# Optimization experiments

Measured on AMD Instinct MI355X. Metric: run time of the kernel, lower is better.

The kernel has to match this reference:

```python
import jax, jax.numpy as jnp
import numpy as np

N_NODES = 100000
N_RELS = 500
N_EDGES = 1000000
IN_DIM = 64
OUT_DIM = 64
BN_EPS = 1e-5


def _bn(v, gamma, beta):
    # BatchNorm1d in training mode: batch mean / biased variance
    m = jnp.mean(v, axis=0)
    var = jnp.var(v, axis=0)
    return (v - m) * jax.lax.rsqrt(var + BN_EPS) * gamma + beta


def setup_inputs() -> dict:
    key = jax.random.key(0)
    ks = jax.random.split(key, 12)
    inp = {
        "x": jax.random.normal(ks[0], (N_NODES, IN_DIM), dtype=jnp.float32),
        "r": jax.random.normal(ks[1], (N_RELS, IN_DIM), dtype=jnp.float32),
        "que_context": jax.random.normal(ks[2], (OUT_DIM,), dtype=jnp.float32),
        "edge_index": jax.random.randint(ks[3], (2, N_EDGES), 0, N_NODES),
        "edge_attr": jax.random.randint(ks[4], (N_EDGES,), 0, N_RELS),
        "edge_type": jax.random.randint(ks[5], (N_EDGES,), 0, N_RELS),
        # mess_trans: Linear(2*in_dim -> out_dim)
        "W_m": jax.random.normal(ks[6], (OUT_DIM, 2 * IN_DIM), dtype=jnp.float32) * 0.05,
        "b_m": jnp.zeros((OUT_DIM,), dtype=jnp.float32),
        # atten_weight: [2*out_dim] (stored as [1, 2*out_dim] in torch)
        "atten_w": jax.random.normal(ks[7], (2 * OUT_DIM,), dtype=jnp.float32) * 0.1,
        # rel_trans: Linear(in_dim -> out_dim)
        "W_r": jax.random.normal(ks[8], (OUT_DIM, IN_DIM), dtype=jnp.float32) * 0.05,
        "b_r": jnp.zeros((OUT_DIM,), dtype=jnp.float32),
        # batchnorm affine params
        "e_gamma": jnp.ones((OUT_DIM,), dtype=jnp.float32),
        "e_beta": jnp.zeros((OUT_DIM,), dtype=jnp.float32),
        "r_gamma": jnp.ones((OUT_DIM,), dtype=jnp.float32),
        "r_beta": jnp.zeros((OUT_DIM,), dtype=jnp.float32),
    }
    return inp


def reference(x, r, que_context, edge_index, edge_attr, edge_type,
              W_m, b_m, atten_w, W_r, b_r, e_gamma, e_beta, r_gamma, r_beta):
    src = edge_index[0]  # [E]
    tgt = edge_index[1]  # [E]

    # gather source-node and edge-relation embeddings, linear message transform
    source_embeds = x[src]            # [E, in_dim]
    edge_rel_embeds = r[edge_attr]    # [E, in_dim]
    messages = jnp.concatenate([source_embeds, edge_rel_embeds], axis=1) @ W_m.T + b_m  # [E, out_dim]

    # edge-wise attention score: <atten_w, [messages ; que_context]>
    # split dot product to avoid materializing the concat
    aw_m, aw_q = atten_w[:OUT_DIM], atten_w[OUT_DIM:]
    atten = messages @ aw_m + jnp.dot(aw_q, que_context)  # [E]
    atten = jnp.exp(jnp.tanh(atten))

    # scatter-sum normalization (softmax-like over incoming edges)
    coeffs_sum = jax.ops.segment_sum(atten, tgt, num_segments=N_NODES)  # [N]
    weights = atten / coeffs_sum[tgt]                                   # [E]

    # weighted scatter-sum aggregation
    x_new = jax.ops.segment_sum(messages * weights[:, None], tgt, num_segments=N_NODES)  # [N, out_dim]
    x_new = jnp.tanh(_bn(x_new, e_gamma, e_beta))  # dropout = identity (eval)

    r_new = jnp.tanh(_bn(r @ W_r.T + b_r, r_gamma, r_beta))
    return (x_new, r_new)
```

## Files before the change

kernel.cpp:

```cpp
#include <hip/hip_runtime.h>
#include <hip/hip_fp16.h>

#define N_NODES 100000
#define N_RELS  500
#define N_EDGES 1000000
#define SRCMASK 131071

#define OFF_C     0
#define OFF_SUMS  64
#define OFF_SUMSQ 128
#define OFF_RSUM  320
#define OFF_RSQ   384
#define OFF_SR    576
#define OFF_RP    1088
#define OFF_SX    33152
#define OFF_DEG   133152
#define OFF_OFF   233216
#define OFF_META  333248
#define OFF_PRH   2333248
#define OFF_PXH   2349280
#define OFF_ACCH  5549280
#define OFF_PART  8749280

typedef _Float16 h8 __attribute__((ext_vector_type(8)));
typedef float f4 __attribute__((ext_vector_type(4)));

__global__ void __launch_bounds__(256) k_rel(const float* __restrict__ r, const float* __restrict__ Wm,
                                             const float* __restrict__ Wr, const float* __restrict__ br,
                                             const float* __restrict__ aw, const float* __restrict__ bm,
                                             const float* __restrict__ que, float* __restrict__ ws) {
    __shared__ float wm[64][65];
    __shared__ float wr[64][65];
    __shared__ float awl[64];
    int tid = threadIdx.x;
    for (int i = tid; i < 4096; i += 256) {
        int row = i >> 6, col = i & 63;
        wm[row][col] = Wm[row * 128 + 64 + col];
        wr[row][col] = Wr[row * 64 + col];
    }
    if (tid < 64) awl[tid] = aw[tid];
    __syncthreads();
    int lane = tid & 63, wv = tid >> 6;
    int i = blockIdx.x * 4 + wv;
    float rv = r[i * 64 + lane];
    float p = 0.f, q = br[lane];
#pragma unroll
    for (int k = 0; k < 64; ++k) {
        float rk = __shfl(rv, k);
        p += wm[lane][k] * rk;
        q += wr[lane][k] * rk;
    }
    __half* prh = (__half*)(ws + OFF_PRH);
    prh[i * 64 + lane] = __float2half(p);
    ws[OFF_RP + i * 64 + lane] = q;
    atomicAdd(&ws[OFF_RSUM + lane], q);
    atomicAdd(&ws[OFF_RSQ + lane], q * q);
    float t = p * awl[lane];
    for (int o = 32; o > 0; o >>= 1) t += __shfl_down(t, o);
    if (lane == 0) ws[OFF_SR + i] = t;
    if (blockIdx.x == 0 && tid < 64) {
        float v = aw[tid] * bm[tid] + aw[64 + tid] * que[tid];
        for (int o = 32; o > 0; o >>= 1) v += __shfl_down(v, o);
        if (tid == 0) ws[OFF_C] = v;
    }
}

__global__ void __launch_bounds__(128) k_px(const float* __restrict__ x, const float* __restrict__ Wm,
                                            const float* __restrict__ aw, float* __restrict__ ws) {
    int tid = threadIdx.x;
    int lane = tid & 63, wv = tid >> 6;
    int wtile = blockIdx.x * 2 + wv;
    int n0 = wtile * 16;
    int rrow = lane & 15, grp = lane >> 4;

    h8 bfr[4][2];
    float awv[4];
#pragma unroll
    for (int ct = 0; ct < 4; ++ct) {
        int col = ct * 16 + rrow;
        awv[ct] = aw[col];
        const float* wp = Wm + col * 128;
#pragma unroll
        for (int h = 0; h < 2; ++h) {
            f4 w0 = *(const f4*)(wp + h * 32 + grp * 8);
            f4 w1 = *(const f4*)(wp + h * 32 + grp * 8 + 4);
            h8 b;
#pragma unroll
            for (int j = 0; j < 4; ++j) { b[j] = (_Float16)w0[j]; b[4 + j] = (_Float16)w1[j]; }
            bfr[ct][h] = b;
        }
    }
    const float* xp = x + (size_t)(n0 + rrow) * 64;
    h8 afr[2];
#pragma unroll
    for (int h = 0; h < 2; ++h) {
        f4 a0 = *(const f4*)(xp + h * 32 + grp * 8);
        f4 a1 = *(const f4*)(xp + h * 32 + grp * 8 + 4);
        h8 a;
#pragma unroll
        for (int j = 0; j < 4; ++j) { a[j] = (_Float16)a0[j]; a[4 + j] = (_Float16)a1[j]; }
        afr[h] = a;
    }
    f4 acc[4];
#pragma unroll
    for (int ct = 0; ct < 4; ++ct) acc[ct] = (f4){0.f, 0.f, 0.f, 0.f};
#pragma unroll
    for (int h = 0; h < 2; ++h)
#pragma unroll
        for (int ct = 0; ct < 4; ++ct)
            acc[ct] = __builtin_amdgcn_mfma_f32_16x16x32_f16(afr[h], bfr[ct][h], acc[ct], 0, 0, 0);

    __half* pxh = (__half*)(ws + OFF_PXH);
#pragma unroll
    for (int q = 0; q < 4; ++q) {
        int node = n0 + grp * 4 + q;
#pragma unroll
        for (int ct = 0; ct < 4; ++ct)
            pxh[(size_t)node * 64 + ct * 16 + rrow] = __float2half(acc[ct][q]);
        float t = acc[0][q] * awv[0] + acc[1][q] * awv[1] + acc[2][q] * awv[2] + acc[3][q] * awv[3];
        t += __shfl_xor(t, 1); t += __shfl_xor(t, 2); t += __shfl_xor(t, 4); t += __shfl_xor(t, 8);
        if (rrow == 0) ws[OFF_SX + node] = t;
    }
}

__global__ void __launch_bounds__(256) k_hist(const int* __restrict__ ei, int* __restrict__ deg) {
    int e = blockIdx.x * 256 + threadIdx.x;
    if (e >= N_EDGES) return;
    atomicAdd(&deg[ei[N_EDGES + e]], 1);
}

__global__ void __launch_bounds__(256) k_scan1(const int* __restrict__ deg, int* __restrict__ off,
                                               int* __restrict__ part) {
    __shared__ int ts[256];
    int tid = threadIdx.x;
    int idx0 = blockIdx.x * 1000 + tid * 4;
    int4 d = make_int4(0, 0, 0, 0);
    if (tid < 250) d = *(const int4*)(deg + idx0);
    int s = d.x + d.y + d.z + d.w;
    ts[tid] = s;
    __syncthreads();
    for (int o = 1; o < 256; o <<= 1) {
        int v = (tid >= o) ? ts[tid - o] : 0;
        __syncthreads();
        ts[tid] += v;
        __syncthreads();
    }
    int excl = ts[tid] - s;
    if (tid < 250) {
        off[idx0] = excl;
        off[idx0 + 1] = excl + d.x;
        off[idx0 + 2] = excl + d.x + d.y;
        off[idx0 + 3] = excl + d.x + d.y + d.z;
    }
    if (tid == 255) part[blockIdx.x] = ts[255];
}

__global__ void __launch_bounds__(128) k_scan2(int* __restrict__ part, int* __restrict__ off) {
    __shared__ int ts[128];
    int tid = threadIdx.x;
    int v = (tid < 100) ? part[tid] : 0;
    ts[tid] = v;
    __syncthreads();
    for (int o = 1; o < 128; o <<= 1) {
        int u = (tid >= o) ? ts[tid - o] : 0;
        __syncthreads();
        ts[tid] += u;
        __syncthreads();
    }
    if (tid < 100) part[tid] = ts[tid] - v;
    if (tid == 127) off[N_NODES] = ts[127];
}

__global__ void __launch_bounds__(256) k_scan3(int* __restrict__ off, const int* __restrict__ part,
                                               int* __restrict__ cursor) {
    int i = blockIdx.x * 256 + threadIdx.x;
    if (i >= N_NODES) return;
    int v = off[i] + part[i / 1000];
    off[i] = v;
    cursor[i] = v;
}

__global__ void __launch_bounds__(256) k_scatter(const int* __restrict__ ei, const int* __restrict__ ea,
                                                 const float* __restrict__ ws, int* __restrict__ cursor,
                                                 uint2* __restrict__ meta) {
    int e = blockIdx.x * 256 + threadIdx.x;
    if (e >= N_EDGES) return;
    int src = ei[e], tgt = ei[N_EDGES + e], at = ea[e];
    float a = __expf(tanhf(ws[OFF_SX + src] + ws[OFF_SR + at] + ws[OFF_C]));
    int pos = atomicAdd(&cursor[tgt], 1);
    meta[pos] = make_uint2(__float_as_uint(a), (unsigned)src | ((unsigned)at << 17));
}

__global__ void __launch_bounds__(256) k_main(const int* __restrict__ off, const uint2* __restrict__ meta,
                                              const float* __restrict__ bm, float* __restrict__ ws) {
    __shared__ float bsum[64], bsq[64];
    int tid = threadIdx.x;
    int lane = tid & 63, wv = tid >> 6;
    if (tid < 64) { bsum[tid] = 0.f; bsq[tid] = 0.f; }
    __syncthreads();
    const __half* pxh = (const __half*)(ws + OFF_PXH);
    const __half* prh = (const __half*)(ws + OFF_PRH);
    __half* acch = (__half*)(ws + OFF_ACCH);
    int ld = lane & 31, hf = lane >> 5;
    float2 bm2 = *(const float2*)(bm + 2 * ld);
    float ls0 = 0.f, ls1 = 0.f, lq0 = 0.f, lq1 = 0.f;
    int t0 = blockIdx.x * 32 + wv * 8;
#pragma unroll 1
    for (int g = 0; g < 8; ++g) {
        int t = t0 + g;
        int s = off[t], e = off[t + 1];
        float ax = 0.f, ay = 0.f, asum = 0.f;
        int i = s;
        for (; i + 8 <= e; i += 8) {
            uint2 m0 = meta[i + 0 + hf], m1 = meta[i + 2 + hf];
            uint2 m2 = meta[i + 4 + hf], m3 = meta[i + 6 + hf];
            float2 p0 = __half22float2(*(const __half2*)(pxh + (size_t)(m0.y & SRCMASK) * 64 + 2 * ld));
            float2 q0 = __half22float2(*(const __half2*)(prh + (m0.y >> 17) * 64 + 2 * ld));
            float2 p1 = __half22float2(*(const __half2*)(pxh + (size_t)(m1.y & SRCMASK) * 64 + 2 * ld));
            float2 q1 = __half22float2(*(const __half2*)(prh + (m1.y >> 17) * 64 + 2 * ld));
            float2 p2 = __half22float2(*(const __half2*)(pxh + (size_t)(m2.y & SRCMASK) * 64 + 2 * ld));
            float2 q2 = __half22float2(*(const __half2*)(prh + (m2.y >> 17) * 64 + 2 * ld));
            float2 p3 = __half22float2(*(const __half2*)(pxh + (size_t)(m3.y & SRCMASK) * 64 + 2 * ld));
            float2 q3 = __half22float2(*(const __half2*)(prh + (m3.y >> 17) * 64 + 2 * ld));
            float a0 = __uint_as_float(m0.x), a1 = __uint_as_float(m1.x);
            float a2 = __uint_as_float(m2.x), a3 = __uint_as_float(m3.x);
            ax += a0 * (p0.x + q0.x) + a1 * (p1.x + q1.x) + a2 * (p2.x + q2.x) + a3 * (p3.x + q3.x);
            ay += a0 * (p0.y + q0.y) + a1 * (p1.y + q1.y) + a2 * (p2.y + q2.y) + a3 * (p3.y + q3.y);
            asum += (a0 + a1) + (a2 + a3);
        }
        for (; i < e; i += 2) {
            int j = i + hf;
            bool valid = j < e;
            uint2 m = meta[valid ? j : (e - 1)];
            float a = valid ? __uint_as_float(m.x) : 0.f;
            float2 p = __half22float2(*(const __half2*)(pxh + (size_t)(m.y & SRCMASK) * 64 + 2 * ld));
            float2 q = __half22float2(*(const __half2*)(prh + (m.y >> 17) * 64 + 2 * ld));
            ax += a * (p.x + q.x);
            ay += a * (p.y + q.y);
            asum += a;
        }
        ax += __shfl_xor(ax, 32);
        ay += __shfl_xor(ay, 32);
        asum += __shfl_xor(asum, 32);
        float vx, vy;
        if (e > s) {
            float inv = 1.f / asum;
            vx = ax * inv + bm2.x;
            vy = ay * inv + bm2.y;
        } else { vx = 0.f; vy = 0.f; }
        if (hf == 0) {
            __half2 h2;
            h2.x = __float2half(vx);
            h2.y = __float2half(vy);
            *(__half2*)(acch + (size_t)t * 64 + 2 * ld) = h2;
        }
        ls0 += vx; lq0 += vx * vx;
        ls1 += vy; lq1 += vy * vy;
    }
    if (hf == 0) {
        atomicAdd(&bsum[2 * ld], ls0);
        atomicAdd(&bsq[2 * ld], lq0);
        atomicAdd(&bsum[2 * ld + 1], ls1);
        atomicAdd(&bsq[2 * ld + 1], lq1);
    }
    __syncthreads();
    if (tid < 64) {
        atomicAdd(&ws[OFF_SUMS + tid], bsum[tid]);
        atomicAdd(&ws[OFF_SUMSQ + tid], bsq[tid]);
    }
}

__global__ void __launch_bounds__(256) k_xout(const float* __restrict__ ws, const float* __restrict__ eg,
                                              const float* __restrict__ eb, const float* __restrict__ rg,
                                              const float* __restrict__ rb, float* __restrict__ out) {
    __shared__ float sc[64], sh[64], rsc[64], rsh[64];
    int tid = threadIdx.x;
    if (tid < 64) {
        float mean = ws[OFF_SUMS + tid] * (1.f / N_NODES);
        float var = ws[OFF_SUMSQ + tid] * (1.f / N_NODES) - mean * mean;
        float s = rsqrtf(var + 1e-5f) * eg[tid];
        sc[tid] = s;
        sh[tid] = eb[tid] - mean * s;
        float rmean = ws[OFF_RSUM + tid] * (1.f / N_RELS);
        float rvar = ws[OFF_RSQ + tid] * (1.f / N_RELS) - rmean * rmean;
        float rs = rsqrtf(rvar + 1e-5f) * rg[tid];
        rsc[tid] = rs;
        rsh[tid] = rb[tid] - rmean * rs;
    }
    __syncthreads();
    int lane = tid & 63, wv = tid >> 6;
    const __half* acch = (const __half*)(ws + OFF_ACCH);
    int base = blockIdx.x * 64;
    for (int it = 0; it < 16; ++it) {
        int t = base + it * 4 + wv;
        if (t < N_NODES) {
            float p = __half2float(acch[(size_t)t * 64 + lane]);
            out[(size_t)t * 64 + lane] = tanhf(p * sc[lane] + sh[lane]);
        }
    }
    if (blockIdx.x < 125) {
        int i = blockIdx.x * 4 + wv;
        float p = ws[OFF_RP + i * 64 + lane];
        out[(size_t)N_NODES * 64 + (size_t)i * 64 + lane] = tanhf(p * rsc[lane] + rsh[lane]);
    }
}

extern "C" void kernel_launch(void* const* d_in, const int* in_sizes, int n_in,
                              void* d_out, int out_size, void* d_ws, size_t ws_size,
                              hipStream_t stream) {
    const float* x   = (const float*)d_in[0];
    const float* r   = (const float*)d_in[1];
    const float* que = (const float*)d_in[2];
    const int*   ei  = (const int*)d_in[3];
    const int*   ea  = (const int*)d_in[4];
    const float* Wm  = (const float*)d_in[6];
    const float* bm  = (const float*)d_in[7];
    const float* aw  = (const float*)d_in[8];
    const float* Wr  = (const float*)d_in[9];
    const float* br  = (const float*)d_in[10];
    const float* eg  = (const float*)d_in[11];
    const float* eb  = (const float*)d_in[12];
    const float* rg  = (const float*)d_in[13];
    const float* rb  = (const float*)d_in[14];
    float* out = (float*)d_out;
    float* ws  = (float*)d_ws;
    int*   deg  = (int*)(ws + OFF_DEG);
    int*   off  = (int*)(ws + OFF_OFF);
    int*   part = (int*)(ws + OFF_PART);
    uint2* meta = (uint2*)(ws + OFF_META);

    hipMemsetAsync(ws + OFF_SUMS, 0, 512 * sizeof(float), stream);
    hipMemsetAsync(deg, 0, (size_t)N_NODES * sizeof(int), stream);

    k_rel<<<125, 256, 0, stream>>>(r, Wm, Wr, br, aw, bm, que, ws);
    k_px<<<3125, 128, 0, stream>>>(x, Wm, aw, ws);
    k_hist<<<(N_EDGES + 255) / 256, 256, 0, stream>>>(ei, deg);
    k_scan1<<<100, 256, 0, stream>>>(deg, off, part);
    k_scan2<<<1, 128, 0, stream>>>(part, off);
    k_scan3<<<(N_NODES + 255) / 256, 256, 0, stream>>>(off, part, deg);
    k_scatter<<<(N_EDGES + 255) / 256, 256, 0, stream>>>(ei, ea, ws, deg, meta);
    k_main<<<3125, 256, 0, stream>>>(off, meta, bm, ws);
    k_xout<<<(N_NODES + 63) / 64, 256, 0, stream>>>(ws, eg, eb, rg, rb, out);
}
```

Baseline: 367.8 us.

## Fold memsets and scan2 into kernels; use 16-lane groups per node in aggregation

Moves the zeroing of deg and the BN sums into k_px, so two memsets go away, and makes k_px run before k_rel so it can do that zeroing. k_scan2 is merged into k_scan3: every block redoes the 100-entry partial scan itself, which removes one launch. k_main now gives each node a 16-lane group that loads 4 halves per edge, replacing the 32-lane split across edge parity, which means 16 nodes are processed at once per block. k_xout gets matching float4 vectorized loads and stores. These changes cut launch overhead and shorten the per-node reduction, at the cost of narrower gathers per edge and less parallelism across edges within each node.

```diff
diff --git a/kernel.cpp b/kernel.cpp
--- a/kernel.cpp
+++ b/kernel.cpp
@@ -25,6 +25,74 @@
 typedef _Float16 h8 __attribute__((ext_vector_type(8)));
 typedef float f4 __attribute__((ext_vector_type(4)));
 
+__device__ __forceinline__ float4 h4tof4(uint2 u) {
+    __half2 a = *(__half2*)&u.x, b = *(__half2*)&u.y;
+    float2 fa = __half22float2(a), fb = __half22float2(b);
+    return make_float4(fa.x, fa.y, fb.x, fb.y);
+}
+
+__global__ void __launch_bounds__(128) k_px(const float* __restrict__ x, const float* __restrict__ Wm,
+                                            const float* __restrict__ aw, float* __restrict__ ws,
+                                            int* __restrict__ deg) {
+    int tid = threadIdx.x;
+    if (tid < 32) deg[blockIdx.x * 32 + tid] = 0;
+    if (blockIdx.x == 0)
+        for (int j = tid; j < 512; j += 128) ws[OFF_SUMS + j] = 0.f;
+    int lane = tid & 63, wv = tid >> 6;
+    int wtile = blockIdx.x * 2 + wv;
+    int n0 = wtile * 16;
+    int rrow = lane & 15, grp = lane >> 4;
+
+    h8 bfr[4][2];
+    float awv[4];
+#pragma unroll
+    for (int ct = 0; ct < 4; ++ct) {
+        int col = ct * 16 + rrow;
+        awv[ct] = aw[col];
+        const float* wp = Wm + col * 128;
+#pragma unroll
+        for (int h = 0; h < 2; ++h) {
+            f4 w0 = *(const f4*)(wp + h * 32 + grp * 8);
+            f4 w1 = *(const f4*)(wp + h * 32 + grp * 8 + 4);
+            h8 b;
+#pragma unroll
+            for (int j = 0; j < 4; ++j) { b[j] = (_Float16)w0[j]; b[4 + j] = (_Float16)w1[j]; }
+            bfr[ct][h] = b;
+        }
+    }
+    const float* xp = x + (size_t)(n0 + rrow) * 64;
+    h8 afr[2];
+#pragma unroll
+    for (int h = 0; h < 2; ++h) {
+        f4 a0 = *(const f4*)(xp + h * 32 + grp * 8);
+        f4 a1 = *(const f4*)(xp + h * 32 + grp * 8 + 4);
+        h8 a;
+#pragma unroll
+        for (int j = 0; j < 4; ++j) { a[j] = (_Float16)a0[j]; a[4 + j] = (_Float16)a1[j]; }
+        afr[h] = a;
+    }
+    f4 acc[4];
+#pragma unroll
+    for (int ct = 0; ct < 4; ++ct) acc[ct] = (f4){0.f, 0.f, 0.f, 0.f};
+#pragma unroll
+    for (int h = 0; h < 2; ++h)
+#pragma unroll
+        for (int ct = 0; ct < 4; ++ct)
+            acc[ct] = __builtin_amdgcn_mfma_f32_16x16x32_f16(afr[h], bfr[ct][h], acc[ct], 0, 0, 0);
+
+    __half* pxh = (__half*)(ws + OFF_PXH);
+#pragma unroll
+    for (int q = 0; q < 4; ++q) {
+        int node = n0 + grp * 4 + q;
+#pragma unroll
+        for (int ct = 0; ct < 4; ++ct)
+            pxh[(size_t)node * 64 + ct * 16 + rrow] = __float2half(acc[ct][q]);
+        float t = acc[0][q] * awv[0] + acc[1][q] * awv[1] + acc[2][q] * awv[2] + acc[3][q] * awv[3];
+        t += __shfl_xor(t, 1); t += __shfl_xor(t, 2); t += __shfl_xor(t, 4); t += __shfl_xor(t, 8);
+        if (rrow == 0) ws[OFF_SX + node] = t;
+    }
+}
+
 __global__ void __launch_bounds__(256) k_rel(const float* __restrict__ r, const float* __restrict__ Wm,
                                              const float* __restrict__ Wr, const float* __restrict__ br,
                                              const float* __restrict__ aw, const float* __restrict__ bm,
@@ -65,64 +133,6 @@
     }
 }
 
-__global__ void __launch_bounds__(128) k_px(const float* __restrict__ x, const float* __restrict__ Wm,
-                                            const float* __restrict__ aw, float* __restrict__ ws) {
-    int tid = threadIdx.x;
-    int lane = tid & 63, wv = tid >> 6;
-    int wtile = blockIdx.x * 2 + wv;
-    int n0 = wtile * 16;
-    int rrow = lane & 15, grp = lane >> 4;
-
-    h8 bfr[4][2];
-    float awv[4];
-#pragma unroll
-    for (int ct = 0; ct < 4; ++ct) {
-        int col = ct * 16 + rrow;
-        awv[ct] = aw[col];
-        const float* wp = Wm + col * 128;
-#pragma unroll
-        for (int h = 0; h < 2; ++h) {
-            f4 w0 = *(const f4*)(wp + h * 32 + grp * 8);
-            f4 w1 = *(const f4*)(wp + h * 32 + grp * 8 + 4);
-            h8 b;
-#pragma unroll
-            for (int j = 0; j < 4; ++j) { b[j] = (_Float16)w0[j]; b[4 + j] = (_Float16)w1[j]; }
-            bfr[ct][h] = b;
-        }
-    }
-    const float* xp = x + (size_t)(n0 + rrow) * 64;
-    h8 afr[2];
-#pragma unroll
-    for (int h = 0; h < 2; ++h) {
-        f4 a0 = *(const f4*)(xp + h * 32 + grp * 8);
-        f4 a1 = *(const f4*)(xp + h * 32 + grp * 8 + 4);
-        h8 a;
-#pragma unroll
-        for (int j = 0; j < 4; ++j) { a[j] = (_Float16)a0[j]; a[4 + j] = (_Float16)a1[j]; }
-        afr[h] = a;
-    }
-    f4 acc[4];
-#pragma unroll
-    for (int ct = 0; ct < 4; ++ct) acc[ct] = (f4){0.f, 0.f, 0.f, 0.f};
-#pragma unroll
-    for (int h = 0; h < 2; ++h)
-#pragma unroll
-        for (int ct = 0; ct < 4; ++ct)
-            acc[ct] = __builtin_amdgcn_mfma_f32_16x16x32_f16(afr[h], bfr[ct][h], acc[ct], 0, 0, 0);
-
-    __half* pxh = (__half*)(ws + OFF_PXH);
-#pragma unroll
-    for (int q = 0; q < 4; ++q) {
-        int node = n0 + grp * 4 + q;
-#pragma unroll
-        for (int ct = 0; ct < 4; ++ct)
-            pxh[(size_t)node * 64 + ct * 16 + rrow] = __float2half(acc[ct][q]);
-        float t = acc[0][q] * awv[0] + acc[1][q] * awv[1] + acc[2][q] * awv[2] + acc[3][q] * awv[3];
-        t += __shfl_xor(t, 1); t += __shfl_xor(t, 2); t += __shfl_xor(t, 4); t += __shfl_xor(t, 8);
-        if (rrow == 0) ws[OFF_SX + node] = t;
-    }
-}
-
 __global__ void __launch_bounds__(256) k_hist(const int* __restrict__ ei, int* __restrict__ deg) {
     int e = blockIdx.x * 256 + threadIdx.x;
     if (e >= N_EDGES) return;
@@ -155,29 +165,28 @@
     if (tid == 255) part[blockIdx.x] = ts[255];
 }
 
-__global__ void __launch_bounds__(128) k_scan2(int* __restrict__ part, int* __restrict__ off) {
-    __shared__ int ts[128];
-    int tid = threadIdx.x;
-    int v = (tid < 100) ? part[tid] : 0;
-    ts[tid] = v;
-    __syncthreads();
-    for (int o = 1; o < 128; o <<= 1) {
-        int u = (tid >= o) ? ts[tid - o] : 0;
-        __syncthreads();
-        ts[tid] += u;
-        __syncthreads();
-    }
-    if (tid < 100) part[tid] = ts[tid] - v;
-    if (tid == 127) off[N_NODES] = ts[127];
-}
-
 __global__ void __launch_bounds__(256) k_scan3(int* __restrict__ off, const int* __restrict__ part,
                                                int* __restrict__ cursor) {
-    int i = blockIdx.x * 256 + threadIdx.x;
-    if (i >= N_NODES) return;
-    int v = off[i] + part[i / 1000];
-    off[i] = v;
-    cursor[i] = v;
+    __shared__ int ts[128];
+    int tid = threadIdx.x;
+    if (tid < 128) ts[tid] = (tid < 100) ? part[tid] : 0;
+    __syncthreads();
+    for (int o = 1; o < 128; o <<= 1) {
+        int v = 0;
+        if (tid < 128 && tid >= o) v = ts[tid - o];
+        __syncthreads();
+        if (tid < 128) ts[tid] += v;
+        __syncthreads();
+    }
+    int i = blockIdx.x * 256 + tid;
+    if (i < N_NODES) {
+        int bg = i / 1000;
+        int base = (bg == 0) ? 0 : ts[bg - 1];
+        int v = off[i] + base;
+        off[i] = v;
+        cursor[i] = v;
+    }
+    if (blockIdx.x == 0 && tid == 0) off[N_NODES] = ts[99];
 }
 
 __global__ void __launch_bounds__(256) k_scatter(const int* __restrict__ ei, const int* __restrict__ ea,
@@ -195,74 +204,80 @@
                                               const float* __restrict__ bm, float* __restrict__ ws) {
     __shared__ float bsum[64], bsq[64];
     int tid = threadIdx.x;
-    int lane = tid & 63, wv = tid >> 6;
     if (tid < 64) { bsum[tid] = 0.f; bsq[tid] = 0.f; }
     __syncthreads();
     const __half* pxh = (const __half*)(ws + OFF_PXH);
     const __half* prh = (const __half*)(ws + OFF_PRH);
     __half* acch = (__half*)(ws + OFF_ACCH);
-    int ld = lane & 31, hf = lane >> 5;
-    float2 bm2 = *(const float2*)(bm + 2 * ld);
-    float ls0 = 0.f, ls1 = 0.f, lq0 = 0.f, lq1 = 0.f;
-    int t0 = blockIdx.x * 32 + wv * 8;
+    int qlane = tid & 15;
+    int quarter = tid >> 4;
+    float4 bm4 = *(const float4*)(bm + 4 * qlane);
+    float ls0 = 0.f, ls1 = 0.f, ls2 = 0.f, ls3 = 0.f;
+    float lq0 = 0.f, lq1 = 0.f, lq2 = 0.f, lq3 = 0.f;
+    int t0 = blockIdx.x * 64 + quarter * 4;
 #pragma unroll 1
-    for (int g = 0; g < 8; ++g) {
+    for (int g = 0; g < 4; ++g) {
         int t = t0 + g;
-        int s = off[t], e = off[t + 1];
-        float ax = 0.f, ay = 0.f, asum = 0.f;
+        bool tv = (t < N_NODES);
+        int s = 0, e = 0;
+        if (tv) { s = off[t]; e = off[t + 1]; }
+        float ax = 0.f, ay = 0.f, az = 0.f, aw_ = 0.f, asum = 0.f;
         int i = s;
-        for (; i + 8 <= e; i += 8) {
-            uint2 m0 = meta[i + 0 + hf], m1 = meta[i + 2 + hf];
-            uint2 m2 = meta[i + 4 + hf], m3 = meta[i + 6 + hf];
-            float2 p0 = __half22float2(*(const __half2*)(pxh + (size_t)(m0.y & SRCMASK) * 64 + 2 * ld));
-            float2 q0 = __half22float2(*(const __half2*)(prh + (m0.y >> 17) * 64 + 2 * ld));
-            float2 p1 = __half22float2(*(const __half2*)(pxh + (size_t)(m1.y & SRCMASK) * 64 + 2 * ld));
-            float2 q1 = __half22float2(*(const __half2*)(prh + (m1.y >> 17) * 64 + 2 * ld));
-            float2 p2 = __half22float2(*(const __half2*)(pxh + (size_t)(m2.y & SRCMASK) * 64 + 2 * ld));
-            float2 q2 = __half22float2(*(const __half2*)(prh + (m2.y >> 17) * 64 + 2 * ld));
-            float2 p3 = __half22float2(*(const __half2*)(pxh + (size_t)(m3.y & SRCMASK) * 64 + 2 * ld));
-            float2 q3 = __half22float2(*(const __half2*)(prh + (m3.y >> 17) * 64 + 2 * ld));
+        for (; i + 2 <= e; i += 2) {
+            uint2 m0 = meta[i], m1 = meta[i + 1];
+            uint2 u0 = *(const uint2*)(pxh + (size_t)(m0.y & SRCMASK) * 64 + 4 * qlane);
+            uint2 r0 = *(const uint2*)(prh + (m0.y >> 17) * 64 + 4 * qlane);
+            uint2 u1 = *(const uint2*)(pxh + (size_t)(m1.y & SRCMASK) * 64 + 4 * qlane);
+            uint2 r1 = *(const uint2*)(prh + (m1.y >> 17) * 64 + 4 * qlane);
             float a0 = __uint_as_float(m0.x), a1 = __uint_as_float(m1.x);
-            float a2 = __uint_as_float(m2.x), a3 = __uint_as_float(m3.x);
-            ax += a0 * (p0.x + q0.x) + a1 * (p1.x + q1.x) + a2 * (p2.x + q2.x) + a3 * (p3.x + q3.x);
-            ay += a0 * (p0.y + q0.y) + a1 * (p1.y + q1.y) + a2 * (p2.y + q2.y) + a3 * (p3.y + q3.y);
-            asum += (a0 + a1) + (a2 + a3);
-        }
-        for (; i < e; i += 2) {
-            int j = i + hf;
-            bool valid = j < e;
-            uint2 m = meta[valid ? j : (e - 1)];
-            float a = valid ? __uint_as_float(m.x) : 0.f;
-            float2 p = __half22float2(*(const __half2*)(pxh + (size_t)(m.y & SRCMASK) * 64 + 2 * ld));
-            float2 q = __half22float2(*(const __half2*)(prh + (m.y >> 17) * 64 + 2 * ld));
-            ax += a * (p.x + q.x);
-            ay += a * (p.y + q.y);
-            asum += a;
-        }
-        ax += __shfl_xor(ax, 32);
-        ay += __shfl_xor(ay, 32);
-        asum += __shfl_xor(asum, 32);
-        float vx, vy;
+            float4 v0 = h4tof4(u0), w0 = h4tof4(r0);
+            float4 v1 = h4tof4(u1), w1 = h4tof4(r1);
+            ax += a0 * (v0.x + w0.x) + a1 * (v1.x + w1.x);
+            ay += a0 * (v0.y + w0.y) + a1 * (v1.y + w1.y);
+            az += a0 * (v0.z + w0.z) + a1 * (v1.z + w1.z);
+            aw_ += a0 * (v0.w + w0.w) + a1 * (v1.w + w1.w);
+            asum += a0 + a1;
+        }
+        if (i < e) {
+            uint2 m0 = meta[i];
+            uint2 u0 = *(const uint2*)(pxh + (size_t)(m0.y & SRCMASK) * 64 + 4 * qlane);
+            uint2 r0 = *(const uint2*)(prh + (m0.y >> 17) * 64 + 4 * qlane);
+            float a0 = __uint_as_float(m0.x);
+            float4 v0 = h4tof4(u0), w0 = h4tof4(r0);
+            ax += a0 * (v0.x + w0.x);
+            ay += a0 * (v0.y + w0.y);
+            az += a0 * (v0.z + w0.z);
+            aw_ += a0 * (v0.w + w0.w);
+            asum += a0;
+        }
+        float4 p;
         if (e > s) {
             float inv = 1.f / asum;
-            vx = ax * inv + bm2.x;
-            vy = ay * inv + bm2.y;
-        } else { vx = 0.f; vy = 0.f; }
-        if (hf == 0) {
-            __half2 h2;
-            h2.x = __float2half(vx);
-            h2.y = __float2half(vy);
-            *(__half2*)(acch + (size_t)t * 64 + 2 * ld) = h2;
-        }
-        ls0 += vx; lq0 += vx * vx;
-        ls1 += vy; lq1 += vy * vy;
-    }
-    if (hf == 0) {
-        atomicAdd(&bsum[2 * ld], ls0);
-        atomicAdd(&bsq[2 * ld], lq0);
-        atomicAdd(&bsum[2 * ld + 1], ls1);
-        atomicAdd(&bsq[2 * ld + 1], lq1);
-    }
+            p = make_float4(ax * inv + bm4.x, ay * inv + bm4.y, az * inv + bm4.z, aw_ * inv + bm4.w);
+        } else {
+            p = make_float4(0.f, 0.f, 0.f, 0.f);
+        }
+        if (tv) {
+            __half2 h0 = __floats2half2_rn(p.x, p.y);
+            __half2 h1 = __floats2half2_rn(p.z, p.w);
+            uint2 st;
+            st.x = *(unsigned*)&h0;
+            st.y = *(unsigned*)&h1;
+            *(uint2*)(acch + (size_t)t * 64 + 4 * qlane) = st;
+        }
+        ls0 += p.x; lq0 += p.x * p.x;
+        ls1 += p.y; lq1 += p.y * p.y;
+        ls2 += p.z; lq2 += p.z * p.z;
+        ls3 += p.w; lq3 += p.w * p.w;
+    }
+    atomicAdd(&bsum[4 * qlane + 0], ls0);
+    atomicAdd(&bsum[4 * qlane + 1], ls1);
+    atomicAdd(&bsum[4 * qlane + 2], ls2);
+    atomicAdd(&bsum[4 * qlane + 3], ls3);
+    atomicAdd(&bsq[4 * qlane + 0], lq0);
+    atomicAdd(&bsq[4 * qlane + 1], lq1);
+    atomicAdd(&bsq[4 * qlane + 2], lq2);
+    atomicAdd(&bsq[4 * qlane + 3], lq3);
     __syncthreads();
     if (tid < 64) {
         atomicAdd(&ws[OFF_SUMS + tid], bsum[tid]);
@@ -288,17 +303,27 @@
         rsh[tid] = rb[tid] - rmean * rs;
     }
     __syncthreads();
-    int lane = tid & 63, wv = tid >> 6;
     const __half* acch = (const __half*)(ws + OFF_ACCH);
-    int base = blockIdx.x * 64;
-    for (int it = 0; it < 16; ++it) {
-        int t = base + it * 4 + wv;
-        if (t < N_NODES) {
-            float p = __half2float(acch[(size_t)t * 64 + lane]);
-            out[(size_t)t * 64 + lane] = tanhf(p * sc[lane] + sh[lane]);
+    int qlane = tid & 15, quarter = tid >> 4;
+    float s0 = sc[4 * qlane], s1 = sc[4 * qlane + 1], s2 = sc[4 * qlane + 2], s3 = sc[4 * qlane + 3];
+    float h0 = sh[4 * qlane], h1 = sh[4 * qlane + 1], h2 = sh[4 * qlane + 2], h3 = sh[4 * qlane + 3];
+    int n0 = blockIdx.x * 64 + quarter * 4;
+#pragma unroll
+    for (int g = 0; g < 4; ++g) {
+        int n = n0 + g;
+        if (n < N_NODES) {
+            uint2 u = *(const uint2*)(acch + (size_t)n * 64 + 4 * qlane);
+            float4 p = h4tof4(u);
+            float4 o;
+            o.x = tanhf(p.x * s0 + h0);
+            o.y = tanhf(p.y * s1 + h1);
+            o.z = tanhf(p.z * s2 + h2);
+            o.w = tanhf(p.w * s3 + h3);
+            *(float4*)(out + (size_t)n * 64 + 4 * qlane) = o;
         }
     }
     if (blockIdx.x < 125) {
+        int lane = tid & 63, wv = tid >> 6;
         int i = blockIdx.x * 4 + wv;
         float p = ws[OFF_RP + i * 64 + lane];
         out[(size_t)N_NODES * 64 + (size_t)i * 64 + lane] = tanhf(p * rsc[lane] + rsh[lane]);
@@ -329,16 +354,12 @@
     int*   part = (int*)(ws + OFF_PART);
     uint2* meta = (uint2*)(ws + OFF_META);
 
-    hipMemsetAsync(ws + OFF_SUMS, 0, 512 * sizeof(float), stream);
-    hipMemsetAsync(deg, 0, (size_t)N_NODES * sizeof(int), stream);
-
+    k_px<<<3125, 128, 0, stream>>>(x, Wm, aw, ws, deg);
     k_rel<<<125, 256, 0, stream>>>(r, Wm, Wr, br, aw, bm, que, ws);
-    k_px<<<3125, 128, 0, stream>>>(x, Wm, aw, ws);
     k_hist<<<(N_EDGES + 255) / 256, 256, 0, stream>>>(ei, deg);
     k_scan1<<<100, 256, 0, stream>>>(deg, off, part);
-    k_scan2<<<1, 128, 0, stream>>>(part, off);
     k_scan3<<<(N_NODES + 255) / 256, 256, 0, stream>>>(off, part, deg);
     k_scatter<<<(N_EDGES + 255) / 256, 256, 0, stream>>>(ei, ea, ws, deg, meta);
-    k_main<<<3125, 256, 0, stream>>>(off, meta, bm, ws);
+    k_main<<<(N_NODES + 63) / 64, 256, 0, stream>>>(off, meta, bm, ws);
     k_xout<<<(N_NODES + 63) / 64, 256, 0, stream>>>(ws, eg, eb, rg, rb, out);
 }
```

New measurement: 319.5 us. 1.15x faster.
